# Kernel tuning notes

Hardware: AMD Instinct MI355X
Metric: run time of the kernel (lower is better)

## Reference

```python
import jax, jax.numpy as jnp
import numpy as np

R = 3                 # corr_radius
G = 2 * R + 1         # 7x7 support grid
LEVELS = 4
C = 128               # latent_dim


def _bilinear(fmap, xs, ys):
    """fmap: [D,H,W]; xs, ys: [...] pixel coords (align_corners=True, zero pad).
    Returns [D, ...]."""
    D, H, W = fmap.shape
    x0 = jnp.floor(xs)
    y0 = jnp.floor(ys)
    wx = xs - x0
    wy = ys - y0
    x0i = x0.astype(jnp.int32)
    y0i = y0.astype(jnp.int32)

    def gather(yi, xi):
        valid = ((xi >= 0) & (xi < W) & (yi >= 0) & (yi < H)).astype(fmap.dtype)
        xc = jnp.clip(xi, 0, W - 1)
        yc = jnp.clip(yi, 0, H - 1)
        return fmap[:, yc, xc] * valid[None]

    v00 = gather(y0i, x0i)
    v01 = gather(y0i, x0i + 1)
    v10 = gather(y0i + 1, x0i)
    v11 = gather(y0i + 1, x0i + 1)
    return (v00 * (1 - wy) * (1 - wx) + v01 * (1 - wy) * wx
            + v10 * wy * (1 - wx) + v11 * wy * wx)


def _corr_feat(fmap_b, coords_l):
    """fmap_b: [B,D,H,W]; coords_l: [B,N,2] (x,y pixel coords at this level).
    Returns [B,N,G,G,D] bilinearly sampled support-grid features."""
    off = jnp.linspace(-R, R, G, dtype=coords_l.dtype)
    ox = jnp.broadcast_to(off[:, None], (G, G))  # offset added to x varies along i
    oy = jnp.broadcast_to(off[None, :], (G, G))  # offset added to y varies along j
    xs = coords_l[..., 0][..., None, None] + ox  # [B,N,G,G]
    ys = coords_l[..., 1][..., None, None] + oy
    feat = jax.vmap(_bilinear)(fmap_b, xs, ys)   # [B,D,N,G,G]
    return jnp.transpose(feat, (0, 2, 3, 4, 1))  # [B,N,G,G,D]


def setup_inputs() -> dict:
    key = jax.random.key(0)
    ks = jax.random.split(key, 16)
    B, N = 1, 4096
    shapes = [(96, 128), (48, 64), (24, 32), (12, 16)]
    inp = {}
    for i, (h, w) in enumerate(shapes):
        inp[f"fmaps{i}"] = jax.random.normal(ks[i], (B, 1, C, h, w), jnp.float32)
        inp[f"tfeat{i}"] = jax.random.normal(ks[4 + i], (B, 1, G * G, N, C), jnp.float32)
    # coords in pixel units at level 0: x in [0, W0-1], y in [0, H0-1]
    u = jax.random.uniform(ks[8], (B, 1, N, 2), jnp.float32)
    inp["coords"] = u * jnp.array([127.0, 95.0], jnp.float32)
    inp["w1"] = jax.random.normal(ks[9], (G * G * G * G, 384), jnp.float32) * 0.02
    inp["b1"] = jnp.zeros((384,), jnp.float32)
    inp["w2"] = jax.random.normal(ks[10], (384, 256), jnp.float32) * 0.02
    inp["b2"] = jnp.zeros((256,), jnp.float32)
    return inp


def reference(fmaps0, fmaps1, fmaps2, fmaps3, coords,
              tfeat0, tfeat1, tfeat2, tfeat3, w1, b1, w2, b2):
    """LiteTracker correlation-pyramid hot path (T = num_new_frames = 1):
    per-level support-grid bilinear gather -> 7x7 x 7x7 correlation volume
    -> corr_mlp (GELU) -> concat over pyramid levels. Returns [B,1,N,1024]."""
    fmaps = [fmaps0, fmaps1, fmaps2, fmaps3]
    tfeats = [tfeat0, tfeat1, tfeat2, tfeat3]
    B, T, N, _ = coords.shape  # T == 1
    coords_init = coords.reshape(B * T, N, 2)

    embs = []
    for i in range(LEVELS):
        fmap_b = fmaps[i][:, 0]                       # [B,D,H,W]
        corr_feat = _corr_feat(fmap_b, coords_init / (2.0 ** i))  # [B,N,G,G,D]
        # template support feats: [B,1,G*G,N,C] -> [B,N,G,G,C]
        tmpl = tfeats[i].reshape(B, G, G, N, C).transpose(0, 3, 1, 2, 4)
        corr_vol = jnp.einsum('bnhwc,bnijc->bnhwij', corr_feat, tmpl)
        x = corr_vol.reshape(B * T * N, G * G * G * G)
        h = jax.nn.gelu(x @ w1 + b1, approximate=False)
        embs.append(h @ w2 + b2)
    corr_embs = jnp.concatenate(embs, axis=-1).reshape(B, T, N, -1)
    return corr_embs
```

## Files before the change

kernel.cpp:

```cpp
#include <hip/hip_runtime.h>


typedef __bf16 bf16x8 __attribute__((ext_vector_type(8)));
typedef float f32x4 __attribute__((ext_vector_type(4)));

#define KPAD 2432
#define K_RAW 2401
#define NPTS 4096

__device__ __forceinline__ float b2f(unsigned short u) {
    return __uint_as_float(((unsigned int)u) << 16);
}
__device__ __forceinline__ unsigned short f2b(float f) {
    unsigned int u = __float_as_uint(f);
    u += 0x7fffu + ((u >> 16) & 1u);
    return (unsigned short)(u >> 16);
}
__device__ __forceinline__ void unpack8(uint4 v, float* f) {
    f[0] = b2f((unsigned short)(v.x & 0xffffu)); f[1] = b2f((unsigned short)(v.x >> 16));
    f[2] = b2f((unsigned short)(v.y & 0xffffu)); f[3] = b2f((unsigned short)(v.y >> 16));
    f[4] = b2f((unsigned short)(v.z & 0xffffu)); f[5] = b2f((unsigned short)(v.z >> 16));
    f[6] = b2f((unsigned short)(v.w & 0xffffu)); f[7] = b2f((unsigned short)(v.w >> 16));
}
__device__ __forceinline__ uint4 pack8(const float* f) {
    unsigned short pk[8];
#pragma unroll
    for (int j = 0; j < 8; ++j) pk[j] = f2b(f[j]);
    uint4 o;
    o.x = pk[0] | ((unsigned int)pk[1] << 16);
    o.y = pk[2] | ((unsigned int)pk[3] << 16);
    o.z = pk[4] | ((unsigned int)pk[5] << 16);
    o.w = pk[6] | ((unsigned int)pk[7] << 16);
    return o;
}

__global__ __launch_bounds__(256) void k_prep(
    const float* __restrict__ f0, const float* __restrict__ f1,
    const float* __restrict__ f2, const float* __restrict__ f3,
    const float* __restrict__ w1, const float* __restrict__ w2,
    unsigned short* __restrict__ fmapT, unsigned short* __restrict__ W1T,
    unsigned short* __restrict__ W2T)
{
    int idx = blockIdx.x * 256 + threadIdx.x;
    const int FT = 2088960;
    if (idx < FT) {
        int off, HW;
        const float* src;
        if (idx < 1572864)      { off = 0;       HW = 12288; src = f0; }
        else if (idx < 1966080) { off = 1572864; HW = 3072;  src = f1; }
        else if (idx < 2064384) { off = 1966080; HW = 768;   src = f2; }
        else                    { off = 2064384; HW = 192;   src = f3; }
        int r = idx - off;
        int c = r / HW, p = r - c * HW;
        fmapT[off + p * 128 + c] = f2b(src[r]);
    } else if (idx < FT + 933888) {
        int j = idx - FT;
        int n = j / KPAD, k = j - n * KPAD;
        W1T[j] = (k < K_RAW) ? f2b(w1[k * 384 + n]) : (unsigned short)0;
    } else if (idx < FT + 933888 + 98304) {
        int j = idx - (FT + 933888);
        int n = j / 384, k = j - n * 384;
        W2T[j] = f2b(w2[k * 256 + n]);
    }
}

__device__ __forceinline__ void corr_body(unsigned short* sm, int bb,
    const unsigned short* __restrict__ fm,
    const float* __restrict__ tf,
    const float* __restrict__ coords,
    unsigned short* __restrict__ X,
    int W, int H, float scale, int n0)
{
    unsigned short* fA = sm;
    unsigned short* fB = sm + 64 * 136;
    const int tid = threadIdx.x;
    const int nl = bb;
    const int n  = n0 + nl;

    const float px = coords[2 * n]     * scale;
    const float py = coords[2 * n + 1] * scale;

    for (int i = tid; i < 2040; i += 256) {
        fA[49 * 136 + i] = 0;
        fB[49 * 136 + i] = 0;
    }
    for (int i = tid; i < 784; i += 256) {
        int g = i >> 4, c8 = i & 15;
        const float* p = tf + (size_t)g * (NPTS * 128) + (size_t)n * 128 + c8 * 8;
        float v[8];
#pragma unroll
        for (int j = 0; j < 8; ++j) v[j] = p[j];
        *reinterpret_cast<uint4*>(&fB[g * 136 + c8 * 8]) = pack8(v);
    }
    for (int i = tid; i < 784; i += 256) {
        int s = i >> 4, c8 = i & 15;
        int a = s / 7, b = s - a * 7;
        float sx = px + (float)(a - 3);
        float sy = py + (float)(b - 3);
        float x0f = floorf(sx), y0f = floorf(sy);
        float wx = sx - x0f, wy = sy - y0f;
        int x0 = (int)x0f, y0 = (int)y0f;
        float acc[8] = {0.f, 0.f, 0.f, 0.f, 0.f, 0.f, 0.f, 0.f};
#pragma unroll
        for (int dy = 0; dy < 2; ++dy) {
            int yi = y0 + dy;
            if (yi < 0 || yi >= H) continue;
            float wyv = dy ? wy : 1.0f - wy;
#pragma unroll
            for (int dx = 0; dx < 2; ++dx) {
                int xi = x0 + dx;
                if (xi < 0 || xi >= W) continue;
                float wv = wyv * (dx ? wx : 1.0f - wx);
                uint4 v = *reinterpret_cast<const uint4*>(
                    fm + (size_t)(yi * W + xi) * 128 + c8 * 8);
                float f[8]; unpack8(v, f);
#pragma unroll
                for (int j = 0; j < 8; ++j) acc[j] += wv * f[j];
            }
        }
        *reinterpret_cast<uint4*>(&fA[s * 136 + c8 * 8]) = pack8(acc);
    }
    unsigned short* Xrow = X + (size_t)nl * KPAD;
    if (tid < 31) Xrow[K_RAW + tid] = 0;
    __syncthreads();

    const int wave = tid >> 6, lane = tid & 63;
    const int la = lane & 15, lq = lane >> 4;
    const int m0 = wave * 16;
    bf16x8 af[4];
#pragma unroll
    for (int kt = 0; kt < 4; ++kt)
        af[kt] = *reinterpret_cast<const bf16x8*>(&fA[(m0 + la) * 136 + kt * 32 + lq * 8]);
#pragma unroll
    for (int nt = 0; nt < 4; ++nt) {
        f32x4 acc = {0.f, 0.f, 0.f, 0.f};
#pragma unroll
        for (int kt = 0; kt < 4; ++kt) {
            bf16x8 bfr = *reinterpret_cast<const bf16x8*>(&fB[(nt * 16 + la) * 136 + kt * 32 + lq * 8]);
            acc = __builtin_amdgcn_mfma_f32_16x16x32_bf16(af[kt], bfr, acc, 0, 0, 0);
        }
#pragma unroll
        for (int r = 0; r < 4; ++r) {
            int m = m0 + lq * 4 + r;
            int nn = nt * 16 + la;
            if (m < 49 && nn < 49) Xrow[m * 49 + nn] = f2b(acc[r]);
        }
    }
}

__device__ __forceinline__ void gemm1_body(unsigned short* sm, int lb,
    const unsigned short* __restrict__ X,
    const unsigned short* __restrict__ W1T,
    const float* __restrict__ b1,
    unsigned short* __restrict__ Hout)
{
    unsigned short* Al = sm;
    unsigned short* Bl = sm + 64 * 40;
    const int tid = threadIdx.x;
    const int bm = lb / 3, bn = lb - bm * 3;
    const int m_base = bm * 64, n_base = bn * 128;

    const int wave = tid >> 6, lane = tid & 63;
    const int wm = wave >> 1, wn = wave & 1;
    const int la = lane & 15, lq = lane >> 4;

    f32x4 acc[2][4];
#pragma unroll
    for (int i = 0; i < 2; ++i)
#pragma unroll
        for (int j = 0; j < 4; ++j) acc[i][j] = {0.f, 0.f, 0.f, 0.f};

    const int a_row = tid >> 2, a_c8 = (tid & 3) * 8;
    for (int k0 = 0; k0 < KPAD; k0 += 32) {
        {
            uint4 v = *reinterpret_cast<const uint4*>(
                X + (size_t)(m_base + a_row) * KPAD + k0 + a_c8);
            *reinterpret_cast<uint4*>(&Al[a_row * 40 + a_c8]) = v;
        }
#pragma unroll
        for (int i = 0; i < 2; ++i) {
            int idx = tid + i * 256;
            int row = idx >> 2, c8 = (idx & 3) * 8;
            uint4 v = *reinterpret_cast<const uint4*>(
                W1T + (size_t)(n_base + row) * KPAD + k0 + c8);
            *reinterpret_cast<uint4*>(&Bl[row * 40 + c8]) = v;
        }
        __syncthreads();
        bf16x8 af[2], bfr[4];
#pragma unroll
        for (int mt = 0; mt < 2; ++mt)
            af[mt] = *reinterpret_cast<const bf16x8*>(&Al[(wm * 32 + mt * 16 + la) * 40 + lq * 8]);
#pragma unroll
        for (int nt = 0; nt < 4; ++nt)
            bfr[nt] = *reinterpret_cast<const bf16x8*>(&Bl[(wn * 64 + nt * 16 + la) * 40 + lq * 8]);
#pragma unroll
        for (int mt = 0; mt < 2; ++mt)
#pragma unroll
            for (int nt = 0; nt < 4; ++nt)
                acc[mt][nt] = __builtin_amdgcn_mfma_f32_16x16x32_bf16(af[mt], bfr[nt], acc[mt][nt], 0, 0, 0);
        __syncthreads();
    }
#pragma unroll
    for (int mt = 0; mt < 2; ++mt) {
#pragma unroll
        for (int nt = 0; nt < 4; ++nt) {
            int nn = n_base + wn * 64 + nt * 16 + la;
            float bias = b1[nn];
#pragma unroll
            for (int r = 0; r < 4; ++r) {
                int m = m_base + wm * 32 + mt * 16 + lq * 4 + r;
                float v = acc[mt][nt][r] + bias;
                v = 0.5f * v * (1.0f + erff(v * 0.70710678118654752f));
                Hout[(size_t)m * 384 + nn] = f2b(v);
            }
        }
    }
}

__device__ __forceinline__ void gemm2_body(unsigned short* sm, int lb,
    const unsigned short* __restrict__ Hin,
    const unsigned short* __restrict__ W2T,
    const float* __restrict__ b2,
    float* __restrict__ out,
    int lvl, int n0)
{
    unsigned short* Al = sm;
    unsigned short* Bl = sm + 64 * 40;
    const int tid = threadIdx.x;
    const int bm = lb >> 1, bn = lb & 1;
    const int m_base = bm * 64, n_base = bn * 128;

    const int wave = tid >> 6, lane = tid & 63;
    const int wm = wave >> 1, wn = wave & 1;
    const int la = lane & 15, lq = lane >> 4;

    f32x4 acc[2][4];
#pragma unroll
    for (int i = 0; i < 2; ++i)
#pragma unroll
        for (int j = 0; j < 4; ++j) acc[i][j] = {0.f, 0.f, 0.f, 0.f};

    const int a_row = tid >> 2, a_c8 = (tid & 3) * 8;
    for (int k0 = 0; k0 < 384; k0 += 32) {
        {
            uint4 v = *reinterpret_cast<const uint4*>(
                Hin + (size_t)(m_base + a_row) * 384 + k0 + a_c8);
            *reinterpret_cast<uint4*>(&Al[a_row * 40 + a_c8]) = v;
        }
#pragma unroll
        for (int i = 0; i < 2; ++i) {
            int idx = tid + i * 256;
            int row = idx >> 2, c8 = (idx & 3) * 8;
            uint4 v = *reinterpret_cast<const uint4*>(
                W2T + (size_t)(n_base + row) * 384 + k0 + c8);
            *reinterpret_cast<uint4*>(&Bl[row * 40 + c8]) = v;
        }
        __syncthreads();
        bf16x8 af[2], bfr[4];
#pragma unroll
        for (int mt = 0; mt < 2; ++mt)
            af[mt] = *reinterpret_cast<const bf16x8*>(&Al[(wm * 32 + mt * 16 + la) * 40 + lq * 8]);
#pragma unroll
        for (int nt = 0; nt < 4; ++nt)
            bfr[nt] = *reinterpret_cast<const bf16x8*>(&Bl[(wn * 64 + nt * 16 + la) * 40 + lq * 8]);
#pragma unroll
        for (int mt = 0; mt < 2; ++mt)
#pragma unroll
            for (int nt = 0; nt < 4; ++nt)
                acc[mt][nt] = __builtin_amdgcn_mfma_f32_16x16x32_bf16(af[mt], bfr[nt], acc[mt][nt], 0, 0, 0);
        __syncthreads();
    }
#pragma unroll
    for (int mt = 0; mt < 2; ++mt) {
#pragma unroll
        for (int nt = 0; nt < 4; ++nt) {
            int nn = n_base + wn * 64 + nt * 16 + la;
            float bias = b2[nn];
#pragma unroll
            for (int r = 0; r < 4; ++r) {
                int m = m_base + wm * 32 + mt * 16 + lq * 4 + r;
                out[(size_t)(n0 + m) * 1024 + lvl * 256 + nn] = acc[mt][nt][r] + bias;
            }
        }
    }
}

__global__ __launch_bounds__(256) void k_stage(
    const unsigned short* __restrict__ fm, const float* __restrict__ tfp,
    const float* __restrict__ coords,
    unsigned short* __restrict__ Xd, int W, int H, float scale, int n0c, int nCorr,
    const unsigned short* __restrict__ Xs, const unsigned short* __restrict__ W1T,
    const float* __restrict__ b1, unsigned short* __restrict__ Hd, int nG1,
    const unsigned short* __restrict__ Hs, const unsigned short* __restrict__ W2T,
    const float* __restrict__ b2, float* __restrict__ out, int lvl2, int n0g2)
{
    __shared__ __align__(16) unsigned short sm[2 * 64 * 136];
    const int bb = blockIdx.x;
    if (bb < nCorr) {
        corr_body(sm, bb, fm, tfp, coords, Xd, W, H, scale, n0c);
    } else if (bb < nCorr + nG1) {
        gemm1_body(sm, bb - nCorr, Xs, W1T, b1, Hd);
    } else {
        gemm2_body(sm, bb - nCorr - nG1, Hs, W2T, b2, out, lvl2, n0g2);
    }
}

extern "C" void kernel_launch(void* const* d_in, const int* in_sizes, int n_in,
                              void* d_out, int out_size, void* d_ws, size_t ws_size,
                              hipStream_t stream)
{
    const float *fm[4], *tf[4], *coords, *w1, *b1, *w2, *b2;
    if (n_in >= 13 && in_sizes[0] == 384) {
        b1 = (const float*)d_in[0]; b2 = (const float*)d_in[1];
        coords = (const float*)d_in[2];
        for (int i = 0; i < 4; ++i) fm[i] = (const float*)d_in[3 + i];
        for (int i = 0; i < 4; ++i) tf[i] = (const float*)d_in[7 + i];
        w1 = (const float*)d_in[11]; w2 = (const float*)d_in[12];
    } else if (n_in >= 13 && in_sizes[1] == 25690112) {
        for (int i = 0; i < 4; ++i) { fm[i] = (const float*)d_in[2 * i];
                                      tf[i] = (const float*)d_in[2 * i + 1]; }
        coords = (const float*)d_in[8];
        w1 = (const float*)d_in[9];  b1 = (const float*)d_in[10];
        w2 = (const float*)d_in[11]; b2 = (const float*)d_in[12];
    } else {
        for (int i = 0; i < 4; ++i) fm[i] = (const float*)d_in[i];
        coords = (const float*)d_in[4];
        for (int i = 0; i < 4; ++i) tf[i] = (const float*)d_in[5 + i];
        w1 = (const float*)d_in[9];  b1 = (const float*)d_in[10];
        w2 = (const float*)d_in[11]; b2 = (const float*)d_in[12];
    }

    const int   cW[4]   = {128, 64, 32, 16};
    const int   cH[4]   = {96, 48, 24, 12};
    const int   cOff[4] = {0, 1572864, 1966080, 2064384};
    const float cS[4]   = {1.0f, 0.5f, 0.25f, 0.125f};

    int CH, nbuf;
    if (ws_size >= (size_t)52379648)      { CH = 4096; nbuf = 2; }
    else if (ws_size >= (size_t)17776640) { CH = 1024; nbuf = 2; }
    else                                  { CH = 1024; nbuf = 1; }

    char* ws = (char*)d_ws;
    size_t xBytes = (size_t)CH * KPAD * 2;
    size_t hBytes = (size_t)CH * 384 * 2;
    size_t off = 0;
    unsigned short* Xb[2]; unsigned short* Hb[2];
    Xb[0] = (unsigned short*)(ws + off); off += xBytes;
    if (nbuf == 2) { Xb[1] = (unsigned short*)(ws + off); off += xBytes; }
    else           { Xb[1] = Xb[0]; }
    Hb[0] = (unsigned short*)(ws + off); off += hBytes;
    if (nbuf == 2) { Hb[1] = (unsigned short*)(ws + off); off += hBytes; }
    else           { Hb[1] = Hb[0]; }
    unsigned short* fmapT = (unsigned short*)(ws + off); off += 4177920;
    unsigned short* W1T   = (unsigned short*)(ws + off); off += 1867776;
    unsigned short* W2T   = (unsigned short*)(ws + off); off += 196608;

    hipLaunchKernelGGL(k_prep, dim3(12192), dim3(256), 0, stream,
                       fm[0], fm[1], fm[2], fm[3], w1, w2, fmapT, W1T, W2T);

    const int S   = (CH == 4096) ? 4 : 16;
    const int nG1 = (CH / 64) * 3;
    const int nG2 = (CH / 64) * 2;

    if (nbuf == 2) {
        for (int t = 0; t < S + 2; ++t) {
            const int s0 = t, s1 = t - 1, s2 = t - 2;
            const int nc = (s0 < S) ? CH : 0;
            const int n1 = (s1 >= 0 && s1 < S) ? nG1 : 0;
            const int n2 = (s2 >= 0 && s2 < S) ? nG2 : 0;
            const int l0 = nc ? ((CH == 4096) ? s0 : (s0 >> 2)) : 0;
            const int l2 = n2 ? ((CH == 4096) ? s2 : (s2 >> 2)) : 0;
            const int n00 = (nc && CH != 4096) ? ((s0 & 3) << 10) : 0;
            const int n02 = (n2 && CH != 4096) ? ((s2 & 3) << 10) : 0;
            hipLaunchKernelGGL(k_stage, dim3(nc + n1 + n2), dim3(256), 0, stream,
                fmapT + cOff[l0], tf[l0], coords,
                Xb[t & 1], cW[l0], cH[l0], cS[l0], n00, nc,
                Xb[(t + 1) & 1], W1T, b1, Hb[(t + 1) & 1], n1,
                Hb[t & 1], W2T, b2, (float*)d_out, l2, n02);
        }
    } else {
        for (int s = 0; s < S; ++s) {
            const int l = s >> 2, n0 = (s & 3) << 10;
            hipLaunchKernelGGL(k_stage, dim3(CH), dim3(256), 0, stream,
                fmapT + cOff[l], tf[l], coords,
                Xb[0], cW[l], cH[l], cS[l], n0, CH,
                Xb[0], W1T, b1, Hb[0], 0,
                Hb[0], W2T, b2, (float*)d_out, l, n0);
            hipLaunchKernelGGL(k_stage, dim3(nG1), dim3(256), 0, stream,
                fmapT, tf[0], coords, Xb[0], 0, 0, 0.f, 0, 0,
                Xb[0], W1T, b1, Hb[0], nG1,
                Hb[0], W2T, b2, (float*)d_out, l, n0);
            hipLaunchKernelGGL(k_stage, dim3(nG2), dim3(256), 0, stream,
                fmapT, tf[0], coords, Xb[0], 0, 0, 0.f, 0, 0,
                Xb[0], W1T, b1, Hb[0], 0,
                Hb[0], W2T, b2, (float*)d_out, l, n0);
        }
    }
}
```

Measured before the change: 702.5 us.

## Stage template feats as swizzled fp32 in LDS, branchless gather, reorder block roles

The corr stage now issues template-feature loads as 16-byte vectors into registers before the bilinear gather. It stores them raw in fp32 into an XOR-swizzled LDS region and converts to bf16 only when building MFMA fragments, which drops the per-element pack and the padding zero-fill. The bilinear gather is made branchless with clamped indices and validity-masked weights, and each thread handles fixed sample slots. Blocks are reordered so GEMM blocks dispatch before corr blocks, shared memory is shrunk, and launch bounds request 4 blocks per CU. This trades extra register pressure and an fp32 LDS footprint for overlapped global loads and higher occupancy.

```diff
diff --git a/kernel.cpp b/kernel.cpp
--- a/kernel.cpp
+++ b/kernel.cpp
@@ -7,6 +7,9 @@
 #define KPAD 2432
 #define K_RAW 2401
 #define NPTS 4096
+
+#define FB_BYTE   13328
+#define SM_SHORTS 19208
 
 __device__ __forceinline__ float b2f(unsigned short u) {
     return __uint_as_float(((unsigned int)u) << 16);
@@ -21,17 +24,6 @@
     f[2] = b2f((unsigned short)(v.y & 0xffffu)); f[3] = b2f((unsigned short)(v.y >> 16));
     f[4] = b2f((unsigned short)(v.z & 0xffffu)); f[5] = b2f((unsigned short)(v.z >> 16));
     f[6] = b2f((unsigned short)(v.w & 0xffffu)); f[7] = b2f((unsigned short)(v.w >> 16));
-}
-__device__ __forceinline__ uint4 pack8(const float* f) {
-    unsigned short pk[8];
-#pragma unroll
-    for (int j = 0; j < 8; ++j) pk[j] = f2b(f[j]);
-    uint4 o;
-    o.x = pk[0] | ((unsigned int)pk[1] << 16);
-    o.y = pk[2] | ((unsigned int)pk[3] << 16);
-    o.z = pk[4] | ((unsigned int)pk[5] << 16);
-    o.w = pk[6] | ((unsigned int)pk[7] << 16);
-    return o;
 }
 
 __global__ __launch_bounds__(256) void k_prep(
@@ -72,59 +64,84 @@
     int W, int H, float scale, int n0)
 {
     unsigned short* fA = sm;
-    unsigned short* fB = sm + 64 * 136;
+    char* fB = (char*)sm + FB_BYTE;
     const int tid = threadIdx.x;
-    const int nl = bb;
-    const int n  = n0 + nl;
+    const int lane = tid & 63, wave = tid >> 6;
+    const int n = n0 + bb;
 
     const float px = coords[2 * n]     * scale;
     const float py = coords[2 * n + 1] * scale;
-
-    for (int i = tid; i < 2040; i += 256) {
-        fA[49 * 136 + i] = 0;
-        fB[49 * 136 + i] = 0;
-    }
-    for (int i = tid; i < 784; i += 256) {
-        int g = i >> 4, c8 = i & 15;
-        const float* p = tf + (size_t)g * (NPTS * 128) + (size_t)n * 128 + c8 * 8;
-        float v[8];
-#pragma unroll
-        for (int j = 0; j < 8; ++j) v[j] = p[j];
-        *reinterpret_cast<uint4*>(&fB[g * 136 + c8 * 8]) = pack8(v);
-    }
-    for (int i = tid; i < 784; i += 256) {
-        int s = i >> 4, c8 = i & 15;
-        int a = s / 7, b = s - a * 7;
-        float sx = px + (float)(a - 3);
-        float sy = py + (float)(b - 3);
-        float x0f = floorf(sx), y0f = floorf(sy);
-        float wx = sx - x0f, wy = sy - y0f;
-        int x0 = (int)x0f, y0 = (int)y0f;
-        float acc[8] = {0.f, 0.f, 0.f, 0.f, 0.f, 0.f, 0.f, 0.f};
-#pragma unroll
-        for (int dy = 0; dy < 2; ++dy) {
-            int yi = y0 + dy;
-            if (yi < 0 || yi >= H) continue;
-            float wyv = dy ? wy : 1.0f - wy;
-#pragma unroll
-            for (int dx = 0; dx < 2; ++dx) {
-                int xi = x0 + dx;
-                if (xi < 0 || xi >= W) continue;
-                float wv = wyv * (dx ? wx : 1.0f - wx);
-                uint4 v = *reinterpret_cast<const uint4*>(
-                    fm + (size_t)(yi * W + xi) * 128 + c8 * 8);
-                float f[8]; unpack8(v, f);
-#pragma unroll
-                for (int j = 0; j < 8; ++j) acc[j] += wv * f[j];
+    const float* tfn = tf + (size_t)n * 128;
+
+    uint4 rv[7];
+#pragma unroll
+    for (int k = 0; k < 7; ++k) {
+        if (k < 6 || tid < 32) {
+            int c = tid + (k << 8);
+            int g = c >> 5;
+            int L = c << 4;
+            rv[k] = *reinterpret_cast<const uint4*>(
+                tfn + (size_t)g * (NPTS * 128) + ((L & 511) >> 2));
+        }
+    }
+
+    const int c8 = lane & 15;
+    const int s_base = wave * 16 + (lane >> 4);
+#pragma unroll
+    for (int k = 0; k < 4; ++k) {
+        int s = s_base + 4 * k;
+        if (s < 49) {
+            int a = s / 7, b = s - a * 7;
+            float sx = px + (float)(a - 3);
+            float sy = py + (float)(b - 3);
+            float x0f = floorf(sx), y0f = floorf(sy);
+            float wx = sx - x0f, wy = sy - y0f;
+            int x0 = (int)x0f, y0 = (int)y0f;
+            int x1 = x0 + 1, y1 = y0 + 1;
+            int xc0 = x0 < 0 ? 0 : (x0 >= W ? W - 1 : x0);
+            int xc1 = x1 < 0 ? 0 : (x1 >= W ? W - 1 : x1);
+            int yc0 = y0 < 0 ? 0 : (y0 >= H ? H - 1 : y0);
+            int yc1 = y1 < 0 ? 0 : (y1 >= H ? H - 1 : y1);
+            float vx0 = (x0 >= 0 && x0 < W) ? 1.f : 0.f;
+            float vx1 = (x1 >= 0 && x1 < W) ? 1.f : 0.f;
+            float vy0 = (y0 >= 0 && y0 < H) ? 1.f : 0.f;
+            float vy1 = (y1 >= 0 && y1 < H) ? 1.f : 0.f;
+            float w00 = (1.f - wy) * (1.f - wx) * vy0 * vx0;
+            float w01 = (1.f - wy) * wx         * vy0 * vx1;
+            float w10 = wy         * (1.f - wx) * vy1 * vx0;
+            float w11 = wy         * wx         * vy1 * vx1;
+            const unsigned short* pb = fm + c8 * 8;
+            uint4 q00 = *reinterpret_cast<const uint4*>(pb + (size_t)(yc0 * W + xc0) * 128);
+            uint4 q01 = *reinterpret_cast<const uint4*>(pb + (size_t)(yc0 * W + xc1) * 128);
+            uint4 q10 = *reinterpret_cast<const uint4*>(pb + (size_t)(yc1 * W + xc0) * 128);
+            uint4 q11 = *reinterpret_cast<const uint4*>(pb + (size_t)(yc1 * W + xc1) * 128);
+            float f00[8], f01[8], f10[8], f11[8];
+            unpack8(q00, f00); unpack8(q01, f01); unpack8(q10, f10); unpack8(q11, f11);
+            bf16x8 r;
+#pragma unroll
+            for (int j = 0; j < 8; ++j) {
+                float v = w00 * f00[j] + w01 * f01[j] + w10 * f10[j] + w11 * f11[j];
+                r[j] = (__bf16)v;
             }
-        }
-        *reinterpret_cast<uint4*>(&fA[s * 136 + c8 * 8]) = pack8(acc);
-    }
-    unsigned short* Xrow = X + (size_t)nl * KPAD;
+            *reinterpret_cast<bf16x8*>(&fA[s * 136 + c8 * 8]) = r;
+        }
+    }
+
+    unsigned short* Xrow = X + (size_t)bb * KPAD;
     if (tid < 31) Xrow[K_RAW + tid] = 0;
+
+#pragma unroll
+    for (int k = 0; k < 7; ++k) {
+        if (k < 6 || tid < 32) {
+            int c = tid + (k << 8);
+            int g = c >> 5;
+            int L = c << 4;
+            int po = L ^ ((g & 7) << 4);
+            *reinterpret_cast<uint4*>(fB + po) = rv[k];
+        }
+    }
     __syncthreads();
 
-    const int wave = tid >> 6, lane = tid & 63;
     const int la = lane & 15, lq = lane >> 4;
     const int m0 = wave * 16;
     bf16x8 af[4];
@@ -133,17 +150,26 @@
         af[kt] = *reinterpret_cast<const bf16x8*>(&fA[(m0 + la) * 136 + kt * 32 + lq * 8]);
 #pragma unroll
     for (int nt = 0; nt < 4; ++nt) {
+        int row = nt * 16 + la;
+        int rowc = row < 49 ? row : 48;
+        int rswz = (rowc & 7) << 4;
         f32x4 acc = {0.f, 0.f, 0.f, 0.f};
 #pragma unroll
         for (int kt = 0; kt < 4; ++kt) {
-            bf16x8 bfr = *reinterpret_cast<const bf16x8*>(&fB[(nt * 16 + la) * 136 + kt * 32 + lq * 8]);
+            int Lb = rowc * 512 + kt * 128 + lq * 32;
+            f32x4 h0 = *reinterpret_cast<const f32x4*>(fB + (Lb ^ rswz));
+            f32x4 h1 = *reinterpret_cast<const f32x4*>(fB + ((Lb + 16) ^ rswz));
+            bf16x8 bfr;
+            bfr[0] = (__bf16)h0[0]; bfr[1] = (__bf16)h0[1];
+            bfr[2] = (__bf16)h0[2]; bfr[3] = (__bf16)h0[3];
+            bfr[4] = (__bf16)h1[0]; bfr[5] = (__bf16)h1[1];
+            bfr[6] = (__bf16)h1[2]; bfr[7] = (__bf16)h1[3];
             acc = __builtin_amdgcn_mfma_f32_16x16x32_bf16(af[kt], bfr, acc, 0, 0, 0);
         }
 #pragma unroll
         for (int r = 0; r < 4; ++r) {
             int m = m0 + lq * 4 + r;
-            int nn = nt * 16 + la;
-            if (m < 49 && nn < 49) Xrow[m * 49 + nn] = f2b(acc[r]);
+            if (m < 49 && row < 49) Xrow[m * 49 + row] = f2b(acc[r]);
         }
     }
 }
@@ -285,23 +311,24 @@
     }
 }
 
-__global__ __launch_bounds__(256) void k_stage(
+__global__ __launch_bounds__(256, 4) void k_stage(
     const unsigned short* __restrict__ fm, const float* __restrict__ tfp,
     const float* __restrict__ coords,
-    unsigned short* __restrict__ Xd, int W, int H, float scale, int n0c, int nCorr,
+    unsigned short* __restrict__ Xd, int W, int H, float scale, int n0c,
     const unsigned short* __restrict__ Xs, const unsigned short* __restrict__ W1T,
     const float* __restrict__ b1, unsigned short* __restrict__ Hd, int nG1,
     const unsigned short* __restrict__ Hs, const unsigned short* __restrict__ W2T,
-    const float* __restrict__ b2, float* __restrict__ out, int lvl2, int n0g2)
-{
-    __shared__ __align__(16) unsigned short sm[2 * 64 * 136];
+    const float* __restrict__ b2, float* __restrict__ out, int lvl2, int n0g2,
+    int nG2)
+{
+    __shared__ __align__(16) unsigned short sm[SM_SHORTS];
     const int bb = blockIdx.x;
-    if (bb < nCorr) {
-        corr_body(sm, bb, fm, tfp, coords, Xd, W, H, scale, n0c);
-    } else if (bb < nCorr + nG1) {
-        gemm1_body(sm, bb - nCorr, Xs, W1T, b1, Hd);
+    if (bb < nG1) {
+        gemm1_body(sm, bb, Xs, W1T, b1, Hd);
+    } else if (bb < nG1 + nG2) {
+        gemm2_body(sm, bb - nG1, Hs, W2T, b2, out, lvl2, n0g2);
     } else {
-        gemm2_body(sm, bb - nCorr - nG1, Hs, W2T, b2, out, lvl2, n0g2);
+        corr_body(sm, bb - nG1 - nG2, fm, tfp, coords, Xd, W, H, scale, n0c);
     }
 }
 
@@ -374,26 +401,26 @@
             const int n02 = (n2 && CH != 4096) ? ((s2 & 3) << 10) : 0;
             hipLaunchKernelGGL(k_stage, dim3(nc + n1 + n2), dim3(256), 0, stream,
                 fmapT + cOff[l0], tf[l0], coords,
-                Xb[t & 1], cW[l0], cH[l0], cS[l0], n00, nc,
+                Xb[t & 1], cW[l0], cH[l0], cS[l0], n00,
                 Xb[(t + 1) & 1], W1T, b1, Hb[(t + 1) & 1], n1,
-                Hb[t & 1], W2T, b2, (float*)d_out, l2, n02);
+                Hb[t & 1], W2T, b2, (float*)d_out, l2, n02, n2);
         }
     } else {
         for (int s = 0; s < S; ++s) {
             const int l = s >> 2, n0 = (s & 3) << 10;
             hipLaunchKernelGGL(k_stage, dim3(CH), dim3(256), 0, stream,
                 fmapT + cOff[l], tf[l], coords,
-                Xb[0], cW[l], cH[l], cS[l], n0, CH,
+                Xb[0], cW[l], cH[l], cS[l], n0,
                 Xb[0], W1T, b1, Hb[0], 0,
-                Hb[0], W2T, b2, (float*)d_out, l, n0);
+                Hb[0], W2T, b2, (float*)d_out, l, n0, 0);
             hipLaunchKernelGGL(k_stage, dim3(nG1), dim3(256), 0, stream,
-                fmapT, tf[0], coords, Xb[0], 0, 0, 0.f, 0, 0,
+                fmapT, tf[0], coords, Xb[0], 0, 0, 0.f, 0,
                 Xb[0], W1T, b1, Hb[0], nG1,
-                Hb[0], W2T, b2, (float*)d_out, l, n0);
+                Hb[0], W2T, b2, (float*)d_out, l, n0, 0);
             hipLaunchKernelGGL(k_stage, dim3(nG2), dim3(256), 0, stream,
-                fmapT, tf[0], coords, Xb[0], 0, 0, 0.f, 0, 0,
+                fmapT, tf[0], coords, Xb[0], 0, 0, 0.f, 0,
                 Xb[0], W1T, b1, Hb[0], 0,
-                Hb[0], W2T, b2, (float*)d_out, l, n0);
-        }
-    }
-}
+                Hb[0], W2T, b2, (float*)d_out, l, n0, nG2);
+        }
+    }
+}
```

After: 661.3 us. 5.9% less time.
